# Kernel tuning notes

Hardware: AMD Instinct MI355X
Metric: run time of the kernel (lower is better)

Reference implementation:

```python
import jax, jax.numpy as jnp
import numpy as np

DIM = 128
NUM_LAYERS = 2
N_LEGO = 50000
N_POINT = 100000
E_LL = 500000
E_PP = 400000
E_LP = 500000
E_PL = 500000


def _seg_softmax(score, seg, n):
    m = jax.ops.segment_max(score, seg, num_segments=n)
    m = jnp.where(jnp.isfinite(m), m, 0.0)
    e = jnp.exp(score - m[seg])
    d = jax.ops.segment_sum(e, seg, num_segments=n)
    return e / (d[seg] + 1e-16)


def _trans_conv(xs, xd, src, dst, Wq, bq, Wk, bk, Wv, bv, Ws, bs):
    # PyG TransformerConv, heads=1, root skip, no edge features
    q = xd @ Wq + bq
    k = xs @ Wk + bk
    v = xs @ Wv + bv
    score = (q[dst] * k[src]).sum(-1) / jnp.sqrt(jnp.asarray(DIM, q.dtype))
    a = _seg_softmax(score, dst, xd.shape[0])
    agg = jax.ops.segment_sum(a[:, None] * v[src], dst, num_segments=xd.shape[0])
    return agg + xd @ Ws + bs


def _gat_conv(xs, xd, src, dst, W, a_src, a_dst, b):
    # PyG GATConv, heads=1, add_self_loops=False, shared lin for src/dst
    hs = xs @ W
    hd = xd @ W
    score = jax.nn.leaky_relu((hs @ a_src)[src] + (hd @ a_dst)[dst], 0.2)
    a = _seg_softmax(score, dst, xd.shape[0])
    return jax.ops.segment_sum(a[:, None] * hs[src], dst, num_segments=xd.shape[0]) + b


def _edge_conv(x, src, dst, W1, b1, W2, b2):
    # PyG EdgeConv: max_j MLP([x_i, x_j - x_i]); BN treated as identity (eval)
    xi = x[dst]
    h = jax.nn.relu(jnp.concatenate([xi, x[src] - xi], axis=-1) @ W1 + b1)
    m = h @ W2 + b2
    agg = jax.ops.segment_max(m, dst, num_segments=x.shape[0])
    return jnp.where(jnp.isfinite(agg), agg, 0.0)


def _forward(x_lego, x_point, tWq, tbq, tWk, tbk, tWv, tbv, tWs, tbs,
             eW1, eb1, eW2, eb2, gW, gAs, gAd, gb,
             ll_src, ll_dst, pp_src, pp_dst, lp_src, lp_dst, pl_src, pl_dst):
    for layer in range(NUM_LAYERS):
        iA = 2 * layer        # first HeteroConv in the stack
        iB = 2 * layer + 1    # second HeteroConv
        i_lp = 2 * layer      # GAT lego->point instance
        i_pl = 2 * layer + 1  # GAT point->lego instance
        # conv A: 4 relations, HeteroConv sum-aggregation per dst type
        lego_a = _trans_conv(x_lego, x_lego, ll_src, ll_dst,
                             tWq[iA], tbq[iA], tWk[iA], tbk[iA], tWv[iA], tbv[iA], tWs[iA], tbs[iA]) \
               + _gat_conv(x_point, x_lego, pl_src, pl_dst, gW[i_pl], gAs[i_pl], gAd[i_pl], gb[i_pl])
        point_a = _edge_conv(x_point, pp_src, pp_dst, eW1[iA], eb1[iA], eW2[iA], eb2[iA]) \
                + _gat_conv(x_lego, x_point, lp_src, lp_dst, gW[i_lp], gAs[i_lp], gAd[i_lp], gb[i_lp])
        # conv B: intra-type relations only
        x_lego = _trans_conv(lego_a, lego_a, ll_src, ll_dst,
                             tWq[iB], tbq[iB], tWk[iB], tbk[iB], tWv[iB], tbv[iB], tWs[iB], tbs[iB])
        x_point = _edge_conv(point_a, pp_src, pp_dst, eW1[iB], eb1[iB], eW2[iB], eb2[iB])
    return x_lego, x_point


def setup_inputs() -> dict:
    key = jax.random.key(0)
    ks = jax.random.split(key, 32)
    NT = 2 * NUM_LAYERS  # conv instances per conv type
    s = np.float32(1.0 / np.sqrt(DIM))
    sh = np.float32(1.0 / np.sqrt(4 * DIM))
    return {
        "x_lego": jax.random.normal(ks[0], (N_LEGO, DIM), jnp.float32),
        "x_point": jax.random.normal(ks[1], (N_POINT, DIM), jnp.float32),
        "tWq": jax.random.normal(ks[2], (NT, DIM, DIM), jnp.float32) * s,
        "tbq": jnp.zeros((NT, DIM), jnp.float32),
        "tWk": jax.random.normal(ks[3], (NT, DIM, DIM), jnp.float32) * s,
        "tbk": jnp.zeros((NT, DIM), jnp.float32),
        "tWv": jax.random.normal(ks[4], (NT, DIM, DIM), jnp.float32) * s,
        "tbv": jnp.zeros((NT, DIM), jnp.float32),
        "tWs": jax.random.normal(ks[5], (NT, DIM, DIM), jnp.float32) * s,
        "tbs": jnp.zeros((NT, DIM), jnp.float32),
        "eW1": jax.random.normal(ks[6], (NT, 2 * DIM, 4 * DIM), jnp.float32) * s,
        "eb1": jnp.zeros((NT, 4 * DIM), jnp.float32),
        "eW2": jax.random.normal(ks[7], (NT, 4 * DIM, DIM), jnp.float32) * sh,
        "eb2": jnp.zeros((NT, DIM), jnp.float32),
        "gW": jax.random.normal(ks[8], (NT, DIM, DIM), jnp.float32) * s,
        "gAs": jax.random.normal(ks[9], (NT, DIM), jnp.float32) * s,
        "gAd": jax.random.normal(ks[10], (NT, DIM), jnp.float32) * s,
        "gb": jnp.zeros((NT, DIM), jnp.float32),
        "ll_src": jax.random.randint(ks[11], (E_LL,), 0, N_LEGO),
        "ll_dst": jax.random.randint(ks[12], (E_LL,), 0, N_LEGO),
        "pp_src": jax.random.randint(ks[13], (E_PP,), 0, N_POINT),
        "pp_dst": jax.random.randint(ks[14], (E_PP,), 0, N_POINT),
        "lp_src": jax.random.randint(ks[15], (E_LP,), 0, N_LEGO),
        "lp_dst": jax.random.randint(ks[16], (E_LP,), 0, N_POINT),
        "pl_src": jax.random.randint(ks[17], (E_PL,), 0, N_POINT),
        "pl_dst": jax.random.randint(ks[18], (E_PL,), 0, N_LEGO),
    }


def reference(x_lego, x_point, tWq, tbq, tWk, tbk, tWv, tbv, tWs, tbs,
              eW1, eb1, eW2, eb2, gW, gAs, gAd, gb,
              ll_src, ll_dst, pp_src, pp_dst, lp_src, lp_dst, pl_src, pl_dst):
    return _forward(x_lego, x_point, tWq, tbq, tWk, tbk, tWv, tbv, tWs, tbs,
                    eW1, eb1, eW2, eb2, gW, gAs, gAd, gb,
                    ll_src, ll_dst, pp_src, pp_dst, lp_src, lp_dst, pl_src, pl_dst)
```

## Files before the change

kernel.cpp:

```cpp
#include <hip/hip_runtime.h>


typedef unsigned int u32;
typedef unsigned short u16;

#define NL 50000
#define NP 100000
#define ELL 500000
#define EPPE 400000
#define ELPE 500000
#define EPLE 500000
#define ENC_NEG_INF 0x007FFFFFu

using bf16x8 = __attribute__((ext_vector_type(8))) short;
using f32x4  = __attribute__((ext_vector_type(4))) float;
using u16x4  = __attribute__((ext_vector_type(4))) unsigned short;

__device__ __forceinline__ float bf2f(u16 h) { return __uint_as_float(((u32)h) << 16); }
__device__ __forceinline__ u16 f2bf(float f) {
    u32 u = __float_as_uint(f);
    u += 0x7FFFu + ((u >> 16) & 1u);
    return (u16)(u >> 16);
}
__device__ __forceinline__ u32 encf(float f) {
    u32 u = __float_as_uint(f);
    return (u & 0x80000000u) ? ~u : (u | 0x80000000u);
}
__device__ __forceinline__ float decf(u32 u) {
    return __uint_as_float((u & 0x80000000u) ? (u ^ 0x80000000u) : ~u);
}

__global__ void k_detect(const u32* __restrict__ x, u32* __restrict__ flag) {
    int lane = threadIdx.x;
    u16 lo = (u16)(x[lane] & 0xFFFFu);
    float a = fabsf(bf2f(lo));
    int inband = (a > 1e-4f && a < 100.f) ? 1 : 0;
    unsigned long long m = __ballot(inband);
    if (lane == 0) flag[0] = (__popcll(m) >= 32) ? 1u : 0u;
}


__global__ __launch_bounds__(256) void k_cast_any(const void* __restrict__ in,
                                                  float* __restrict__ out, int n,
                                                  const u32* __restrict__ flag) {
    int i = blockIdx.x * 256 + threadIdx.x;
    if (i >= n) return;
    if (flag[0]) out[i] = bf2f(((const u16*)in)[i]);
    else         out[i] = ((const float*)in)[i];
}

__global__ __launch_bounds__(256) void k_store_out(const float* __restrict__ in,
                                                   void* __restrict__ out, size_t off, int n,
                                                   const u32* __restrict__ flag) {
    int i = blockIdx.x * 256 + threadIdx.x;
    if (i >= n) return;
    if (flag[0]) ((u16*)out)[off + i] = f2bf(in[i]);
    else         ((float*)out)[off + i] = in[i];
}

__global__ __launch_bounds__(256) void k_fill_u32(u32* __restrict__ p, u32 v, int n) {
    int i = blockIdx.x * 256 + threadIdx.x;
    if (i < n) p[i] = v;
}

__global__ void k_add128(const float* __restrict__ a, const float* __restrict__ b,
                         float* __restrict__ o) {
    int t = threadIdx.x;
    o[t] = a[t] + b[t];
}

__global__ __launch_bounds__(256) void k_tcast(const float* __restrict__ in,
                                               u16* __restrict__ out,
                                               int K, int N, int total) {
    int i = blockIdx.x * 256 + threadIdx.x;
    if (i >= total) return;
    int per = K * N;
    int c = i / per, r = i - c * per;
    int k = r / N, n = r - k * N;
    out[(size_t)c * per + (size_t)n * K + k] = f2bf(in[i]);
}

__global__ __launch_bounds__(256) void k_w1mod(float* __restrict__ w, int total) {
    int i = blockIdx.x * 256 + threadIdx.x;
    if (i >= total) return;
    int c = i >> 16;
    int r = (i >> 9) & 127;
    int col = i & 511;
    float* base = w + c * 131072;
    base[r * 512 + col] -= base[(r + 128) * 512 + col];
}

__global__ __launch_bounds__(256) void k_split(const float4* __restrict__ x,
                                               u16x4* __restrict__ xh,
                                               u16x4* __restrict__ xl, int n4) {
    int i = blockIdx.x * 256 + threadIdx.x;
    if (i >= n4) return;
    float4 f = x[i];
    float fv[4] = {f.x, f.y, f.z, f.w};
    u16x4 h, l;
#pragma unroll
    for (int j = 0; j < 4; ++j) {
        u16 hi = f2bf(fv[j]);
        h[j] = hi;
        l[j] = f2bf(fv[j] - bf2f(hi));
    }
    xh[i] = h; xl[i] = l;
}

__global__ void k_matvec2(const float* __restrict__ W, const float* __restrict__ a0,
                          const float* __restrict__ a1, float* __restrict__ o) {
    __shared__ float as[128];
    const float* a = blockIdx.x ? a1 : a0;
    int t = threadIdx.x;
    as[t] = a[t];
    __syncthreads();
    float s = 0.f;
#pragma unroll 8
    for (int i = 0; i < 128; ++i) s += W[t * 128 + i] * as[i];
    o[blockIdx.x * 128 + t] = s;
}

__global__ __launch_bounds__(256) void k_node_scalar(const float* __restrict__ X,
                                                     const float* __restrict__ wv,
                                                     float* __restrict__ s, int n) {
    int wid = (blockIdx.x * 256 + threadIdx.x) >> 6;
    int lane = threadIdx.x & 63;
    if (wid >= n) return;
    const float* xr = X + (size_t)wid * 128;
    float v = xr[lane] * wv[lane] + xr[lane + 64] * wv[lane + 64];
#pragma unroll
    for (int o = 32; o; o >>= 1) v += __shfl_xor(v, o);
    if (lane == 0) s[wid] = v;
}


__global__ __launch_bounds__(256) void k_deg(const int* __restrict__ dst,
                                             int* __restrict__ deg, int E) {
    int i = blockIdx.x * 256 + threadIdx.x;
    if (i < E) atomicAdd(deg + dst[i], 1);
}

__global__ __launch_bounds__(256) void k_scan1(const int* __restrict__ deg,
                                               int* __restrict__ rp,
                                               int* __restrict__ aux, int n) {
    __shared__ int ls[256];
    int t = threadIdx.x;
    int i = blockIdx.x * 256 + t;
    int v = (i < n) ? deg[i] : 0;
    ls[t] = v;
    __syncthreads();
#pragma unroll
    for (int off = 1; off < 256; off <<= 1) {
        int a = (t >= off) ? ls[t - off] : 0;
        __syncthreads();
        ls[t] += a;
        __syncthreads();
    }
    if (i < n) rp[i] = ls[t] - v;
    if (t == 255) aux[blockIdx.x] = ls[255];
}

__global__ __launch_bounds__(512) void k_scan2(int* __restrict__ aux, int nb) {
    __shared__ int ls[512];
    int t = threadIdx.x;
    int v = (t < nb) ? aux[t] : 0;
    ls[t] = v;
    __syncthreads();
#pragma unroll
    for (int off = 1; off < 512; off <<= 1) {
        int a = (t >= off) ? ls[t - off] : 0;
        __syncthreads();
        ls[t] += a;
        __syncthreads();
    }
    if (t < nb) aux[t] = ls[t] - v;
}

__global__ __launch_bounds__(256) void k_scan3(int* __restrict__ rp,
                                               const int* __restrict__ aux,
                                               int n, int E) {
    int i = blockIdx.x * 256 + threadIdx.x;
    if (i > n) return;
    if (i == n) rp[n] = E;
    else        rp[i] += aux[i >> 8];
}

__global__ __launch_bounds__(256) void k_copy_i32(const int* __restrict__ a,
                                                  int* __restrict__ b, int n) {
    int i = blockIdx.x * 256 + threadIdx.x;
    if (i < n) b[i] = a[i];
}

__global__ __launch_bounds__(256) void k_scat(const int* __restrict__ src,
                                              const int* __restrict__ dst,
                                              int* __restrict__ cur,
                                              int* __restrict__ col, int E) {
    int i = blockIdx.x * 256 + threadIdx.x;
    if (i >= E) return;
    int pos = atomicAdd(cur + dst[i], 1);
    col[pos] = src[i];
}


__global__ __launch_bounds__(256) void k_attn_trans(const float* __restrict__ Tq,
                                                    const float* __restrict__ Tk,
                                                    const float* __restrict__ Tv,
                                                    const int* __restrict__ rp,
                                                    const int* __restrict__ col,
                                                    float* __restrict__ out, int nd) {
    int row = (blockIdx.x * 256 + threadIdx.x) >> 6;
    int lane = threadIdx.x & 63;
    if (row >= nd) return;
    int e0 = rp[row], e1 = rp[row + 1];
    if (e0 >= e1) return;
    const float* q = Tq + (size_t)row * 128;
    float q0 = q[lane], q1 = q[lane + 64];
    float m = -3.0e38f, l = 0.f, o0 = 0.f, o1 = 0.f;
    for (int e = e0; e < e1; ++e) {
        int s = col[e];
        const float* kr = Tk + (size_t)s * 128;
        float d = q0 * kr[lane] + q1 * kr[lane + 64];
#pragma unroll
        for (int off = 32; off; off >>= 1) d += __shfl_xor(d, off);
        d *= 0.08838834764831845f;
        float mn = fmaxf(m, d);
        float al = expf(m - mn);
        float p  = expf(d - mn);
        const float* vr = Tv + (size_t)s * 128;
        l  = l * al + p;
        o0 = o0 * al + p * vr[lane];
        o1 = o1 * al + p * vr[lane + 64];
        m = mn;
    }
    float inv = 1.f / (l + 1e-16f);
    size_t base = (size_t)row * 128;
    out[base + lane]      += o0 * inv;
    out[base + lane + 64] += o1 * inv;
}

__global__ __launch_bounds__(256) void k_attn_gat(const float* __restrict__ hs,
                                                  const float* __restrict__ ss,
                                                  const float* __restrict__ sd,
                                                  const int* __restrict__ rp,
                                                  const int* __restrict__ col,
                                                  float* __restrict__ out, int nd) {
    int row = (blockIdx.x * 256 + threadIdx.x) >> 6;
    int lane = threadIdx.x & 63;
    if (row >= nd) return;
    int e0 = rp[row], e1 = rp[row + 1];
    if (e0 >= e1) return;
    float sdv = sd[row];
    float m = -3.0e38f, l = 0.f, o0 = 0.f, o1 = 0.f;
    for (int e = e0; e < e1; ++e) {
        int s = col[e];
        float sc = ss[s] + sdv;
        sc = sc > 0.f ? sc : 0.2f * sc;
        float mn = fmaxf(m, sc);
        float al = expf(m - mn);
        float p  = expf(sc - mn);
        const float* hr = hs + (size_t)s * 128;
        l  = l * al + p;
        o0 = o0 * al + p * hr[lane];
        o1 = o1 * al + p * hr[lane + 64];
        m = mn;
    }
    float inv = 1.f / (l + 1e-16f);
    size_t base = (size_t)row * 128;
    out[base + lane]      += o0 * inv;
    out[base + lane + 64] += o1 * inv;
}

#define LSTR 40

__global__ __launch_bounds__(256) void k_mgemm(const float* __restrict__ A_,
                                               const u16* __restrict__ Wt,
                                               const float* __restrict__ bias,
                                               float* __restrict__ Cout,
                                               int M, int N, int K) {
    __shared__ u16 Ahs[128 * LSTR];
    __shared__ u16 Als[128 * LSTR];
    __shared__ u16 Bss[128 * LSTR];
    const int tid = threadIdx.x;
    const int m0 = blockIdx.y * 128, n0 = blockIdx.x * 128;

    const int srow = tid >> 1, sseg = (tid & 1) * 16;
    int arow = m0 + srow;
    if (arow >= M) arow = M - 1;
    const float* Af = A_ + (size_t)arow * K + sseg;
    u16* AhW = &Ahs[srow * LSTR + sseg];
    u16* AlW = &Als[srow * LSTR + sseg];
    const u16* Bp = Wt + (size_t)(n0 + srow) * K + sseg;
    u16* BsW = &Bss[srow * LSTR + sseg];

    const int lane = tid & 63, wv = tid >> 6;
    const int mw = (wv >> 1) * 64, nw = (wv & 1) * 64;
    const int fm = lane & 15, fq = lane >> 4;
    const u16* aRh = &Ahs[(mw + fm) * LSTR + fq * 8];
    const u16* aRl = &Als[(mw + fm) * LSTR + fq * 8];
    const u16* bR  = &Bss[(nw + fm) * LSTR + fq * 8];

    f32x4 acc[4][4];
#pragma unroll
    for (int i = 0; i < 4; ++i)
#pragma unroll
        for (int j = 0; j < 4; ++j) { acc[i][j][0]=0.f; acc[i][j][1]=0.f; acc[i][j][2]=0.f; acc[i][j][3]=0.f; }

    for (int k0 = 0; k0 < K; k0 += 32) {
        __syncthreads();
        float4 f0 = *(const float4*)(Af + k0);
        float4 f1 = *(const float4*)(Af + k0 + 4);
        float4 f2 = *(const float4*)(Af + k0 + 8);
        float4 f3 = *(const float4*)(Af + k0 + 12);
        float v[16] = {f0.x,f0.y,f0.z,f0.w, f1.x,f1.y,f1.z,f1.w,
                       f2.x,f2.y,f2.z,f2.w, f3.x,f3.y,f3.z,f3.w};
        u32 hp[8], lp[8];
#pragma unroll
        for (int i = 0; i < 8; ++i) {
            float x0 = v[2 * i], x1 = v[2 * i + 1];
            u16 h0 = f2bf(x0), h1 = f2bf(x1);
            u16 l0 = f2bf(x0 - bf2f(h0)), l1 = f2bf(x1 - bf2f(h1));
            hp[i] = (u32)h0 | ((u32)h1 << 16);
            lp[i] = (u32)l0 | ((u32)l1 << 16);
        }
        uint4 h04 = {hp[0], hp[1], hp[2], hp[3]}, h48 = {hp[4], hp[5], hp[6], hp[7]};
        uint4 l04 = {lp[0], lp[1], lp[2], lp[3]}, l48 = {lp[4], lp[5], lp[6], lp[7]};
        *(uint4*)AhW = h04; *(uint4*)(AhW + 8) = h48;
        *(uint4*)AlW = l04; *(uint4*)(AlW + 8) = l48;
        *(uint4*)BsW       = *(const uint4*)(Bp + k0);
        *(uint4*)(BsW + 8) = *(const uint4*)(Bp + k0 + 8);
        __syncthreads();

        bf16x8 ah[4], al[4], bfr[4];
#pragma unroll
        for (int i = 0; i < 4; ++i) ah[i]  = *(const bf16x8*)(aRh + i * 16 * LSTR);
#pragma unroll
        for (int i = 0; i < 4; ++i) al[i]  = *(const bf16x8*)(aRl + i * 16 * LSTR);
#pragma unroll
        for (int j = 0; j < 4; ++j) bfr[j] = *(const bf16x8*)(bR + j * 16 * LSTR);
#pragma unroll
        for (int i = 0; i < 4; ++i)
#pragma unroll
            for (int j = 0; j < 4; ++j) {
                acc[i][j] = __builtin_amdgcn_mfma_f32_16x16x32_bf16(ah[i], bfr[j],
                                                                    acc[i][j], 0, 0, 0);
                acc[i][j] = __builtin_amdgcn_mfma_f32_16x16x32_bf16(al[i], bfr[j],
                                                                    acc[i][j], 0, 0, 0);
            }
    }

    float bb[4];
#pragma unroll
    for (int j = 0; j < 4; ++j)
        bb[j] = bias ? bias[n0 + nw + j * 16 + fm] : 0.f;
#pragma unroll
    for (int i = 0; i < 4; ++i) {
#pragma unroll
        for (int reg = 0; reg < 4; ++reg) {
            int r = m0 + mw + i * 16 + fq * 4 + reg;
            if (r >= M) continue;
#pragma unroll
            for (int j = 0; j < 4; ++j)
                Cout[(size_t)r * N + n0 + nw + j * 16 + fm] = acc[i][j][reg] + bb[j];
        }
    }
}

#define HST 72
#define W1ST 264

__global__ __launch_bounds__(512, 4) void k_edge_fused(const u16* __restrict__ Xh,
                                                       const u16* __restrict__ Xl,
                                                       const int* __restrict__ esrc,
                                                       const int* __restrict__ edst,
                                                       const u16* __restrict__ W1t,
                                                       const float* __restrict__ b1,
                                                       const u16* __restrict__ W2t,
                                                       u32* __restrict__ agg, int E) {
    __shared__ u16 W1s[64 * W1ST];
    __shared__ u16 Hh[8 * 16 * HST];
    __shared__ u16 Hl[8 * 16 * HST];
    const int tid = threadIdx.x;
    const int lane = tid & 63, wv = tid >> 6;
    const int fm = lane & 15, fq = lane >> 4;
    const int e0 = blockIdx.x * 128;

    int eo = e0 + wv * 16 + fm;
    if (eo >= E) eo = E - 1;
    const size_t ndof = (size_t)edst[eo] * 128, nsof = (size_t)esrc[eo] * 128;

    bf16x8 xdh[4], xdl[4], xsh[4], xsl[4];
#pragma unroll
    for (int t = 0; t < 4; ++t) {
        int c = t * 32 + fq * 8;
        xdh[t] = *(const bf16x8*)(Xh + ndof + c);
        xdl[t] = *(const bf16x8*)(Xl + ndof + c);
        xsh[t] = *(const bf16x8*)(Xh + nsof + c);
        xsl[t] = *(const bf16x8*)(Xl + nsof + c);
    }

    int erow[4];
#pragma unroll
    for (int r = 0; r < 4; ++r) {
        int e = e0 + wv * 16 + fq * 4 + r;
        erow[r] = (e < E) ? edst[e] : -1;
    }

    f32x4 macc[8];
#pragma unroll
    for (int of = 0; of < 8; ++of) { macc[of][0]=0.f; macc[of][1]=0.f; macc[of][2]=0.f; macc[of][3]=0.f; }

    const int s_row = tid >> 3, s_col = (tid & 7) * 32;
    const u16* w1g = W1t + (size_t)s_row * 256 + s_col;
    u16* w1l = &W1s[s_row * W1ST + s_col];

    const int lbase = (wv * 16 + fm) * HST;

    for (int nc = 0; nc < 8; ++nc) {
        __syncthreads();
        {
            const u16* g = w1g + (size_t)nc * 64 * 256;
#pragma unroll
            for (int j = 0; j < 4; ++j)
                *(uint4*)(w1l + j * 8) = *(const uint4*)(g + j * 8);
        }
        __syncthreads();

        f32x4 hacc[4];
#pragma unroll
        for (int i = 0; i < 4; ++i) { hacc[i][0]=0.f; hacc[i][1]=0.f; hacc[i][2]=0.f; hacc[i][3]=0.f; }

        const u16* w1p = &W1s[fm * W1ST + fq * 8];
#pragma unroll
        for (int t = 0; t < 8; ++t) {
            bf16x8 xh = (t < 4) ? xdh[t] : xsh[t - 4];
            bf16x8 xl = (t < 4) ? xdl[t] : xsl[t - 4];
#pragma unroll
            for (int i = 0; i < 4; ++i) {
                bf16x8 w1 = *(const bf16x8*)(w1p + i * 16 * W1ST + t * 32);
                hacc[i] = __builtin_amdgcn_mfma_f32_16x16x32_bf16(w1, xh, hacc[i], 0, 0, 0);
                hacc[i] = __builtin_amdgcn_mfma_f32_16x16x32_bf16(w1, xl, hacc[i], 0, 0, 0);
            }
        }

        asm volatile("s_waitcnt lgkmcnt(0)" ::: "memory");
#pragma unroll
        for (int i = 0; i < 4; ++i) {
            float4 bb = *(const float4*)(b1 + nc * 64 + i * 16 + fq * 4);
            const float bv[4] = {bb.x, bb.y, bb.z, bb.w};
            u16 hi[4], lo[4];
#pragma unroll
            for (int r = 0; r < 4; ++r) {
                float h = hacc[i][r] + bv[r];
                h = h > 0.f ? h : 0.f;
                hi[r] = f2bf(h);
                lo[r] = f2bf(h - bf2f(hi[r]));
            }
            uint2 ph = {(u32)hi[0] | ((u32)hi[1] << 16), (u32)hi[2] | ((u32)hi[3] << 16)};
            uint2 pl = {(u32)lo[0] | ((u32)lo[1] << 16), (u32)lo[2] | ((u32)lo[3] << 16)};
            *(uint2*)&Hh[lbase + i * 16 + fq * 4] = ph;
            *(uint2*)&Hl[lbase + i * 16 + fq * 4] = pl;
        }
        asm volatile("s_waitcnt lgkmcnt(0)" ::: "memory");

#pragma unroll
        for (int kk = 0; kk < 2; ++kk) {
            bf16x8 ah = *(const bf16x8*)&Hh[lbase + kk * 32 + fq * 8];
            bf16x8 al = *(const bf16x8*)&Hl[lbase + kk * 32 + fq * 8];
            const u16* w2p = W2t + (size_t)fm * 512 + nc * 64 + kk * 32 + fq * 8;
#pragma unroll
            for (int of = 0; of < 8; ++of) {
                bf16x8 w2 = *(const bf16x8*)(w2p + (size_t)of * 16 * 512);
                macc[of] = __builtin_amdgcn_mfma_f32_16x16x32_bf16(ah, w2, macc[of], 0, 0, 0);
                macc[of] = __builtin_amdgcn_mfma_f32_16x16x32_bf16(al, w2, macc[of], 0, 0, 0);
            }
        }
    }

#pragma unroll
    for (int r = 0; r < 4; ++r) {
        if (erow[r] < 0) continue;
        u32* base = agg + (size_t)erow[r] * 128 + fm;
#pragma unroll
        for (int of = 0; of < 8; ++of)
            atomicMax(base + of * 16, encf(macc[of][r]));
    }
}

__global__ __launch_bounds__(256) void k_decode(u32* __restrict__ agg,
                                                const float* __restrict__ b2,
                                                const float* __restrict__ gb, int n) {
    int i = blockIdx.x * 256 + threadIdx.x;
    if (i >= n) return;
    int c = i & 127;
    u32 u = agg[i];
    float v = (u == ENC_NEG_INF) ? 0.f : (decf(u) + b2[c]);
    if (gb) v += gb[c];
    ((float*)agg)[i] = v;
}


extern "C" void kernel_launch(void* const* d_in, const int* in_sizes, int n_in,
                              void* d_out, int out_size, void* d_ws, size_t ws_size,
                              hipStream_t stream) {
    (void)in_sizes; (void)out_size;
    if (n_in < 26) return;
    if (ws_size < (size_t)240000000) return;

    const void* in_xl  = d_in[0];
    const void* in_xp  = d_in[1];
    const void* in_tWq = d_in[2];
    const void* in_tbq = d_in[3];
    const void* in_tWk = d_in[4];
    const void* in_tbk = d_in[5];
    const void* in_tWv = d_in[6];
    const void* in_tbv = d_in[7];
    const void* in_tWs = d_in[8];
    const void* in_tbs = d_in[9];
    const void* in_eW1 = d_in[10];
    const void* in_eb1 = d_in[11];
    const void* in_eW2 = d_in[12];
    const void* in_eb2 = d_in[13];
    const void* in_gW  = d_in[14];
    const void* in_gAs = d_in[15];
    const void* in_gAd = d_in[16];
    const void* in_gb  = d_in[17];
    const int* ll_src = (const int*)d_in[18];
    const int* ll_dst = (const int*)d_in[19];
    const int* pp_src = (const int*)d_in[20];
    const int* pp_dst = (const int*)d_in[21];
    const int* lp_src = (const int*)d_in[22];
    const int* lp_dst = (const int*)d_in[23];
    const int* pl_src = (const int*)d_in[24];
    const int* pl_dst = (const int*)d_in[25];

    char* w = (char*)d_ws;
    auto alloc = [&](size_t bytes) -> char* {
        char* p = w;
        w += (bytes + 255) & ~(size_t)255;
        return p;
    };
    float* XL   = (float*)alloc((size_t)NL * 128 * 4);
    float* XP   = (float*)alloc((size_t)NP * 128 * 4);
    float* LA   = (float*)alloc((size_t)NL * 128 * 4);
    float* PA   = (float*)alloc((size_t)NP * 128 * 4);
    float* ssrc = (float*)alloc((size_t)NP * 4);
    float* sdst = (float*)alloc((size_t)NP * 4);
    float* wv2  = (float*)alloc(256 * 4);
    float* comb = (float*)alloc(128 * 4);
    u32*  dflag = (u32*)  alloc(256);
    float* tbqf = (float*)alloc(512 * 4);
    float* tbkf = (float*)alloc(512 * 4);
    float* tbvf = (float*)alloc(512 * 4);
    float* tbsf = (float*)alloc(512 * 4);
    float* eb1f = (float*)alloc(2048 * 4);
    float* eb2f = (float*)alloc(512 * 4);
    float* gWf  = (float*)alloc(65536 * 4);
    float* gAsf = (float*)alloc(512 * 4);
    float* gAdf = (float*)alloc(512 * 4);
    float* gbf  = (float*)alloc(512 * 4);
    u16* tWqt = (u16*)alloc(65536 * 2);
    u16* tWkt = (u16*)alloc(65536 * 2);
    u16* tWvt = (u16*)alloc(65536 * 2);
    u16* tWst = (u16*)alloc(65536 * 2);
    u16* gWt  = (u16*)alloc(65536 * 2);
    u16* eW1t = (u16*)alloc(524288 * 2);
    u16* eW2t = (u16*)alloc(262144 * 2);
    int* rp_ll  = (int*)alloc((NL + 1) * 4);
    int* rp_lp  = (int*)alloc((NP + 1) * 4);
    int* rp_pl  = (int*)alloc((NL + 1) * 4);
    int* col_ll = (int*)alloc((size_t)ELL * 4);
    int* col_lp = (int*)alloc((size_t)ELPE * 4);
    int* col_pl = (int*)alloc((size_t)EPLE * 4);
    char* U = alloc(76800000);
    float* tWqf = (float*)U;
    float* tWkf = tWqf + 65536;
    float* tWvf = tWkf + 65536;
    float* tWsf = tWvf + 65536;
    float* eW1f = tWsf + 65536;
    float* eW2f = eW1f + 524288;
    float* Tq  = (float*)U;
    float* Tk  = Tq + (size_t)NL * 128;
    float* Tv  = Tk + (size_t)NL * 128;
    float* Ghs = (float*)U;
    u16* Xph = (u16*)U;
    u16* Xpl = Xph + (size_t)NP * 128;

    k_detect<<<1, 64, 0, stream>>>((const u32*)in_xl, dflag);

    auto cast = [&](const void* s_, float* d_, int n) {
        k_cast_any<<<(n + 255) / 256, 256, 0, stream>>>(s_, d_, n, dflag);
    };
    auto fillu = [&](void* p, u32 v, int n) {
        k_fill_u32<<<(n + 255) / 256, 256, 0, stream>>>((u32*)p, v, n);
    };
    auto tcast = [&](const float* s_, u16* d_, int K, int N, int nconv) {
        int total = nconv * K * N;
        k_tcast<<<(total + 255) / 256, 256, 0, stream>>>(s_, d_, K, N, total);
    };

    cast(in_xl, XL, NL * 128);
    cast(in_xp, XP, NP * 128);
    cast(in_tWq, tWqf, 65536); cast(in_tbq, tbqf, 512);
    cast(in_tWk, tWkf, 65536); cast(in_tbk, tbkf, 512);
    cast(in_tWv, tWvf, 65536); cast(in_tbv, tbvf, 512);
    cast(in_tWs, tWsf, 65536); cast(in_tbs, tbsf, 512);
    cast(in_eW1, eW1f, 524288); cast(in_eb1, eb1f, 2048);
    cast(in_eW2, eW2f, 262144); cast(in_eb2, eb2f, 512);
    cast(in_gW, gWf, 65536);
    cast(in_gAs, gAsf, 512); cast(in_gAd, gAdf, 512); cast(in_gb, gbf, 512);

    k_w1mod<<<(262144 + 255) / 256, 256, 0, stream>>>(eW1f, 262144);

    tcast(tWqf, tWqt, 128, 128, 4);
    tcast(tWkf, tWkt, 128, 128, 4);
    tcast(tWvf, tWvt, 128, 128, 4);
    tcast(tWsf, tWst, 128, 128, 4);
    tcast(gWf,  gWt,  128, 128, 4);
    tcast(eW1f, eW1t, 256, 512, 4);
    tcast(eW2f, eW2t, 512, 128, 4);

    int* deg = (int*)U;
    int* cur = deg + NP + 64;
    int* aux = cur + NP + 64;
    auto build_csr = [&](const int* src, const int* dst, int E, int nd,
                         int* rp, int* col) {
        int nb = (nd + 255) / 256;
        fillu(deg, 0u, nd);
        k_deg<<<(E + 255) / 256, 256, 0, stream>>>(dst, deg, E);
        k_scan1<<<nb, 256, 0, stream>>>(deg, rp, aux, nd);
        k_scan2<<<1, 512, 0, stream>>>(aux, nb);
        k_scan3<<<(nd + 256) / 256, 256, 0, stream>>>(rp, aux, nd, E);
        k_copy_i32<<<(nd + 255) / 256, 256, 0, stream>>>(rp, cur, nd);
        k_scat<<<(E + 255) / 256, 256, 0, stream>>>(src, dst, cur, col, E);
    };
    build_csr(ll_src, ll_dst, ELL, NL, rp_ll, col_ll);
    build_csr(lp_src, lp_dst, ELPE, NP, rp_lp, col_lp);
    build_csr(pl_src, pl_dst, EPLE, NL, rp_pl, col_pl);

    auto mgemm = [&](const float* A, const u16* Wt, const float* b, float* C,
                     int M, int N, int K) {
        dim3 g(N / 128, (M + 127) / 128);
        k_mgemm<<<g, 256, 0, stream>>>(A, Wt, b, C, M, N, K);
    };

    auto trans_agg = [&](const float* Xin, float* out, int conv) {
        mgemm(Xin, tWqt + conv * 16384, tbqf + conv * 128, Tq, NL, 128, 128);
        mgemm(Xin, tWkt + conv * 16384, tbkf + conv * 128, Tk, NL, 128, 128);
        mgemm(Xin, tWvt + conv * 16384, tbvf + conv * 128, Tv, NL, 128, 128);
        k_attn_trans<<<(NL + 3) / 4, 256, 0, stream>>>(Tq, Tk, Tv, rp_ll, col_ll,
                                                       out, NL);
    };
    auto gat_conv = [&](const float* Xs, int ns, int nd,
                        const float* Xd, const int* rp, const int* col,
                        int g, float* out) {
        k_matvec2<<<2, 128, 0, stream>>>(gWf + g * 16384, gAsf + g * 128,
                                         gAdf + g * 128, wv2);
        k_node_scalar<<<(ns * 64 + 255) / 256, 256, 0, stream>>>(Xs, wv2, ssrc, ns);
        k_node_scalar<<<(nd * 64 + 255) / 256, 256, 0, stream>>>(Xd, wv2 + 128, sdst, nd);
        mgemm(Xs, gWt + g * 16384, nullptr, Ghs, ns, 128, 128);
        k_attn_gat<<<(nd + 3) / 4, 256, 0, stream>>>(Ghs, ssrc, sdst, rp, col,
                                                     out, nd);
    };
    auto edge_conv = [&](const float* Xin, float* Xout, int conv, const float* gbext) {
        k_split<<<(NP * 32 + 255) / 256, 256, 0, stream>>>(
            (const float4*)Xin, (u16x4*)Xph, (u16x4*)Xpl, NP * 32);
        fillu(Xout, ENC_NEG_INF, NP * 128);
        k_edge_fused<<<(EPPE + 127) / 128, 512, 0, stream>>>(
            Xph, Xpl, pp_src, pp_dst,
            eW1t + conv * 131072, eb1f + conv * 512, eW2t + conv * 65536,
            (u32*)Xout, EPPE);
        k_decode<<<(NP * 128 + 255) / 256, 256, 0, stream>>>((u32*)Xout, eb2f + conv * 128,
                                                             gbext, NP * 128);
    };

    for (int layer = 0; layer < 2; ++layer) {
        int cA = 2 * layer, cB = cA + 1;
        int g_lp = 2 * layer, g_pl = 2 * layer + 1;

        k_add128<<<1, 128, 0, stream>>>(tbsf + cA * 128, gbf + g_pl * 128, comb);
        mgemm(XL, tWst + cA * 16384, comb, LA, NL, 128, 128);
        trans_agg(XL, LA, cA);
        gat_conv(XP, NP, NL, XL, rp_pl, col_pl, g_pl, LA);

        edge_conv(XP, PA, cA, gbf + g_lp * 128);
        gat_conv(XL, NL, NP, XP, rp_lp, col_lp, g_lp, PA);

        mgemm(LA, tWst + cB * 16384, tbsf + cB * 128, XL, NL, 128, 128);
        trans_agg(LA, XL, cB);
        edge_conv(PA, XP, cB, nullptr);
    }

    k_store_out<<<(NL * 128 + 255) / 256, 256, 0, stream>>>(XL, d_out, 0, NL * 128, dflag);
    k_store_out<<<(NP * 128 + 255) / 256, 256, 0, stream>>>(XP, d_out, (size_t)NL * 128,
                                                            NP * 128, dflag);
}
```

Measured before the change: 4.730 ms.

## Replace LDS round-trip of hidden activations with lane shuffles and fragment-ordered W1

The edge MLP kernel no longer writes the ReLU hidden tile to shared memory and reads it back in MFMA A-operand layout. Instead it transposes the accumulator fragments in registers using two xor-shuffles (32 and 16). W1 is now staged in LDS in per-lane fragment order, so each MFMA operand read is a contiguous conflict-free 16-byte load. Shared memory use drops from the padded W1 plus Hh/Hl buffers to a single 32 KB array, which may allow more blocks per CU. In exchange it adds shuffle instructions and select logic.

```diff
diff --git a/kernel.cpp b/kernel.cpp
--- a/kernel.cpp
+++ b/kernel.cpp
@@ -365,8 +365,6 @@
     }
 }
 
-#define HST 72
-#define W1ST 264
 
 __global__ __launch_bounds__(512, 4) void k_edge_fused(const u16* __restrict__ Xh,
                                                        const u16* __restrict__ Xl,
@@ -376,12 +374,11 @@
                                                        const float* __restrict__ b1,
                                                        const u16* __restrict__ W2t,
                                                        u32* __restrict__ agg, int E) {
-    __shared__ u16 W1s[64 * W1ST];
-    __shared__ u16 Hh[8 * 16 * HST];
-    __shared__ u16 Hl[8 * 16 * HST];
+    __shared__ u16 W1f[16384];
     const int tid = threadIdx.x;
     const int lane = tid & 63, wv = tid >> 6;
     const int fm = lane & 15, fq = lane >> 4;
+    const int aBit = fq >> 1, bBit = fq & 1;
     const int e0 = blockIdx.x * 128;
 
     int eo = e0 + wv * 16 + fm;
@@ -409,19 +406,14 @@
 #pragma unroll
     for (int of = 0; of < 8; ++of) { macc[of][0]=0.f; macc[of][1]=0.f; macc[of][2]=0.f; macc[of][3]=0.f; }
 
-    const int s_row = tid >> 3, s_col = (tid & 7) * 32;
-    const u16* w1g = W1t + (size_t)s_row * 256 + s_col;
-    u16* w1l = &W1s[s_row * W1ST + s_col];
-
-    const int lbase = (wv * 16 + fm) * HST;
+    u16* w1l = &W1f[(size_t)(wv * 64 + lane) * 8];
 
     for (int nc = 0; nc < 8; ++nc) {
         __syncthreads();
-        {
-            const u16* g = w1g + (size_t)nc * 64 * 256;
-#pragma unroll
-            for (int j = 0; j < 4; ++j)
-                *(uint4*)(w1l + j * 8) = *(const uint4*)(g + j * 8);
+#pragma unroll
+        for (int m = 0; m < 4; ++m) {
+            const u16* g = W1t + (size_t)(nc * 64 + m * 16 + fm) * 256 + wv * 32 + fq * 8;
+            *(uint4*)(w1l + (size_t)m * 512 * 8) = *(const uint4*)g;
         }
         __syncthreads();
 
@@ -429,20 +421,19 @@
 #pragma unroll
         for (int i = 0; i < 4; ++i) { hacc[i][0]=0.f; hacc[i][1]=0.f; hacc[i][2]=0.f; hacc[i][3]=0.f; }
 
-        const u16* w1p = &W1s[fm * W1ST + fq * 8];
 #pragma unroll
         for (int t = 0; t < 8; ++t) {
             bf16x8 xh = (t < 4) ? xdh[t] : xsh[t - 4];
             bf16x8 xl = (t < 4) ? xdl[t] : xsl[t - 4];
 #pragma unroll
             for (int i = 0; i < 4; ++i) {
-                bf16x8 w1 = *(const bf16x8*)(w1p + i * 16 * W1ST + t * 32);
+                bf16x8 w1 = *(const bf16x8*)&W1f[(size_t)((i * 8 + t) * 64 + lane) * 8];
                 hacc[i] = __builtin_amdgcn_mfma_f32_16x16x32_bf16(w1, xh, hacc[i], 0, 0, 0);
                 hacc[i] = __builtin_amdgcn_mfma_f32_16x16x32_bf16(w1, xl, hacc[i], 0, 0, 0);
             }
         }
 
-        asm volatile("s_waitcnt lgkmcnt(0)" ::: "memory");
+        u32 Wh[4][2], Wl[4][2];
 #pragma unroll
         for (int i = 0; i < 4; ++i) {
             float4 bb = *(const float4*)(b1 + nc * 64 + i * 16 + fq * 4);
@@ -455,17 +446,53 @@
                 hi[r] = f2bf(h);
                 lo[r] = f2bf(h - bf2f(hi[r]));
             }
-            uint2 ph = {(u32)hi[0] | ((u32)hi[1] << 16), (u32)hi[2] | ((u32)hi[3] << 16)};
-            uint2 pl = {(u32)lo[0] | ((u32)lo[1] << 16), (u32)lo[2] | ((u32)lo[3] << 16)};
-            *(uint2*)&Hh[lbase + i * 16 + fq * 4] = ph;
-            *(uint2*)&Hl[lbase + i * 16 + fq * 4] = pl;
+            Wh[i][0] = (u32)hi[0] | ((u32)hi[1] << 16);
+            Wh[i][1] = (u32)hi[2] | ((u32)hi[3] << 16);
+            Wl[i][0] = (u32)lo[0] | ((u32)lo[1] << 16);
+            Wl[i][1] = (u32)lo[2] | ((u32)lo[3] << 16);
         }
-        asm volatile("s_waitcnt lgkmcnt(0)" ::: "memory");
+
+        u32 Rh[2][2][2], Rl[2][2][2];
+#pragma unroll
+        for (int w4 = 0; w4 < 2; ++w4)
+#pragma unroll
+            for (int p = 0; p < 2; ++p) {
+                {
+                    u32 own0 = Wh[2 * w4][p], own1 = Wh[2 * w4 + 1][p];
+                    u32 send = aBit ? own0 : own1;
+                    u32 recv = (u32)__shfl_xor((int)send, 32);
+                    u32 keep = aBit ? own1 : own0;
+                    u32 A0 = aBit ? recv : keep;
+                    u32 A1 = aBit ? keep : recv;
+                    u32 send2 = bBit ? A0 : A1;
+                    u32 recv2 = (u32)__shfl_xor((int)send2, 16);
+                    u32 keep2 = bBit ? A1 : A0;
+                    Rh[w4][0][p] = bBit ? recv2 : keep2;
+                    Rh[w4][1][p] = bBit ? keep2 : recv2;
+                }
+                {
+                    u32 own0 = Wl[2 * w4][p], own1 = Wl[2 * w4 + 1][p];
+                    u32 send = aBit ? own0 : own1;
+                    u32 recv = (u32)__shfl_xor((int)send, 32);
+                    u32 keep = aBit ? own1 : own0;
+                    u32 A0 = aBit ? recv : keep;
+                    u32 A1 = aBit ? keep : recv;
+                    u32 send2 = bBit ? A0 : A1;
+                    u32 recv2 = (u32)__shfl_xor((int)send2, 16);
+                    u32 keep2 = bBit ? A1 : A0;
+                    Rl[w4][0][p] = bBit ? recv2 : keep2;
+                    Rl[w4][1][p] = bBit ? keep2 : recv2;
+                }
+            }
 
 #pragma unroll
         for (int kk = 0; kk < 2; ++kk) {
-            bf16x8 ah = *(const bf16x8*)&Hh[lbase + kk * 32 + fq * 8];
-            bf16x8 al = *(const bf16x8*)&Hl[lbase + kk * 32 + fq * 8];
+            union { u32 u[4]; bf16x8 v; } ch, cl;
+            ch.u[0] = Rh[kk][0][0]; ch.u[1] = Rh[kk][0][1];
+            ch.u[2] = Rh[kk][1][0]; ch.u[3] = Rh[kk][1][1];
+            cl.u[0] = Rl[kk][0][0]; cl.u[1] = Rl[kk][0][1];
+            cl.u[2] = Rl[kk][1][0]; cl.u[3] = Rl[kk][1][1];
+            bf16x8 ah = ch.v, al = cl.v;
             const u16* w2p = W2t + (size_t)fm * 512 + nc * 64 + kk * 32 + fq * 8;
 #pragma unroll
             for (int of = 0; of < 8; ++of) {
```

Measured after the change: 5.019 ms. 1.06x slower.
